# Kernel optimization log

Measured on AMD Instinct MI355X. Metric: run time of the kernel, lower is better.

Reference implementation:

```python
import jax, jax.numpy as jnp
import numpy as np

N = 50000      # nodes
F_IN = 500     # in_channels
MID = 64       # mid_layer_channel
H = 2          # heads
OUT = 40       # out_channels
E = 800000     # edges per order
ORDER = 3
NEG_SLOPE = 0.2


def _gat(x, edge_index, W, a_src, a_dst, b, concat):
    # PyG-style GATConv (eval mode, dropout off), with self loops.
    n = x.shape[0]
    heads, ch = a_src.shape
    h = (x @ W).reshape(n, heads, ch)                    # [N,H,C]
    loop = jnp.arange(n)
    src = jnp.concatenate([edge_index[0], loop])
    dst = jnp.concatenate([edge_index[1], loop])
    al_s = jnp.sum(h * a_src, axis=-1)                   # [N,H]
    al_d = jnp.sum(h * a_dst, axis=-1)                   # [N,H]
    e = jax.nn.leaky_relu(al_s[src] + al_d[dst], NEG_SLOPE)   # [Etot,H]
    m = jax.ops.segment_max(e, dst, num_segments=n)      # softmax over incoming edges per dst
    ex = jnp.exp(e - m[dst])
    den = jax.ops.segment_sum(ex, dst, num_segments=n)
    alpha = ex / (den[dst] + 1e-16)
    out = jax.ops.segment_sum(alpha[:, :, None] * h[src], dst, num_segments=n)  # [N,H,C]
    if concat:
        return out.reshape(n, heads * ch) + b
    return out.mean(axis=1) + b


def _aggr(states, Wmix, wfin):
    # NOrderAggrConv (depth=2): mix order states with [order,order] weights + ELU,
    # then reduce to a single state with a learned [order] combination.
    h = jnp.stack(states, axis=1)                        # [N,order,C]
    h = jax.nn.elu(jnp.einsum('nkc,kj->njc', h, Wmix))
    return jnp.einsum('nkc,k->nc', h, wfin)


def setup_inputs():
    key = jax.random.key(0)
    ks = jax.random.split(key, 40)
    d = {}
    d['node_feature'] = jax.random.normal(ks[0], (N, F_IN), jnp.float32)
    for o in range(ORDER):
        d[f'adj{o}'] = jax.random.randint(ks[1 + o], (2, E), 0, N)
    i = 4
    s = 0.05
    layer_dims = [(F_IN, MID, H * MID), (MID * H, OUT, OUT)]
    for l, (fin, c, bdim) in enumerate(layer_dims):
        for o in range(ORDER):
            d[f'W_{l}_{o}'] = jax.random.normal(ks[i], (fin, H * c), jnp.float32) * s; i += 1
            d[f'as_{l}_{o}'] = jax.random.normal(ks[i], (H, c), jnp.float32) * s; i += 1
            d[f'ad_{l}_{o}'] = jax.random.normal(ks[i], (H, c), jnp.float32) * s; i += 1
            d[f'b_{l}_{o}'] = jnp.zeros((bdim,), jnp.float32)
    for l in range(2):
        d[f'agg{l}_W'] = jax.random.normal(ks[i], (ORDER, ORDER), jnp.float32) * 0.5; i += 1
        d[f'agg{l}_w'] = jnp.full((ORDER,), 1.0 / ORDER, jnp.float32)
    return d


def reference(node_feature, adj0, adj1, adj2,
              W_0_0, as_0_0, ad_0_0, b_0_0,
              W_0_1, as_0_1, ad_0_1, b_0_1,
              W_0_2, as_0_2, ad_0_2, b_0_2,
              W_1_0, as_1_0, ad_1_0, b_1_0,
              W_1_1, as_1_1, ad_1_1, b_1_1,
              W_1_2, as_1_2, ad_1_2, b_1_2,
              agg0_W, agg0_w, agg1_W, agg1_w):
    adjs = (adj0, adj1, adj2)
    p0 = ((W_0_0, as_0_0, ad_0_0, b_0_0),
          (W_0_1, as_0_1, ad_0_1, b_0_1),
          (W_0_2, as_0_2, ad_0_2, b_0_2))
    p1 = ((W_1_0, as_1_0, ad_1_0, b_1_0),
          (W_1_1, as_1_1, ad_1_1, b_1_1),
          (W_1_2, as_1_2, ad_1_2, b_1_2))
    aggs = ((agg0_W, agg0_w), (agg1_W, agg1_w))
    x = node_feature  # eval mode: dropout is identity
    for l, params in enumerate((p0, p1)):
        concat = (l == 0)
        states = [jax.nn.elu(_gat(x, adjs[o], *params[o], concat)) for o in range(ORDER)]
        x = _aggr(states, *aggs[l])
    return jax.nn.log_softmax(x, axis=1)
```

## Files before the change

### kernel.cpp

```cpp
#include <hip/hip_runtime.h>
#include <cstdint>
#include <cstddef>
#include <math.h>


typedef __attribute__((ext_vector_type(8))) short short8;
typedef __attribute__((ext_vector_type(4))) float f32x4;
typedef __attribute__((ext_vector_type(2))) float f32x2;

struct P3f { const float* p[3]; };
struct P3c { const int* p[3]; };

#define SSEG 8
#define SEGSH 17

__device__ __forceinline__ float leakyf(float x) { return x > 0.f ? x : 0.2f * x; }
__device__ __forceinline__ float eluf(float x)   { return x > 0.f ? x : expm1f(x); }

__device__ __forceinline__ unsigned short bf16r(float x) {
  unsigned int u = __float_as_uint(x);
  u += 0x7fffu + ((u >> 16) & 1u);
  return (unsigned short)(u >> 16);
}
__device__ __forceinline__ float bflo(unsigned int u) { return __uint_as_float(u << 16); }
__device__ __forceinline__ float bfhi(unsigned int u) { return __uint_as_float(u & 0xffff0000u); }

__device__ __forceinline__ void bf8_fma2(uint4 q, float xx, f32x2* a) {
  f32x2 v0 = {bflo(q.x), bfhi(q.x)};
  f32x2 v1 = {bflo(q.y), bfhi(q.y)};
  f32x2 v2 = {bflo(q.z), bfhi(q.z)};
  f32x2 v3 = {bflo(q.w), bfhi(q.w)};
  a[0] += xx * v0;
  a[1] += xx * v1;
  a[2] += xx * v2;
  a[3] += xx * v3;
}

__global__ __launch_bounds__(256) void zero_int_kernel(int* p, int n) {
  int i = blockIdx.x * blockDim.x + threadIdx.x;
  if (i < n) p[i] = 0;
}

__global__ __launch_bounds__(256) void convA_kernel(const float* __restrict__ A,
    unsigned short* __restrict__ Ab, int M, int K, int Kpad) {
  int i = blockIdx.x * blockDim.x + threadIdx.x;
  int row = i >> 6;
  int koff = (i & 63) * 8;
  if (row >= M) return;
  const float* ap = A + (size_t)row * K;
  unsigned short v[8];
  if (koff + 8 <= K) {
    float4 q0 = ((const float4*)(ap + koff))[0];
    float4 q1 = ((const float4*)(ap + koff))[1];
    v[0] = bf16r(q0.x); v[1] = bf16r(q0.y); v[2] = bf16r(q0.z); v[3] = bf16r(q0.w);
    v[4] = bf16r(q1.x); v[5] = bf16r(q1.y); v[6] = bf16r(q1.z); v[7] = bf16r(q1.w);
  } else {
#pragma unroll
    for (int k = 0; k < 8; ++k)
      v[k] = (koff + k < K) ? bf16r(ap[koff + k]) : (unsigned short)0;
  }
  *(uint4*)(Ab + (size_t)row * Kpad + koff) = *(const uint4*)v;
}

__global__ __launch_bounds__(256) void count3_kernel(P3c adj,
    int* __restrict__ segcnt, int* __restrict__ posb, int E, int N) {
  int i = blockIdx.x * blockDim.x + threadIdx.x;
  int o = blockIdx.y;
  if (i < E) {
    int d = adj.p[o][E + i];
    int s = i >> SEGSH;
    if (s > SSEG - 1) s = SSEG - 1;
    posb[(size_t)o * E + i] = atomicAdd(&segcnt[((size_t)o * SSEG + s) * N + d], 1);
  }
}

__global__ __launch_bounds__(256) void nodeseg_scan_kernel(int* __restrict__ segcnt,
    int* __restrict__ cntb, int N) {
  int n = blockIdx.x * blockDim.x + threadIdx.x;
  int o = blockIdx.y;
  if (n >= N) return;
  int run = 0;
#pragma unroll
  for (int s = 0; s < SSEG; ++s) {
    size_t idx = ((size_t)o * SSEG + s) * N + n;
    int c = segcnt[idx];
    segcnt[idx] = run;
    run += c;
  }
  cntb[o * N + n] = run;
}

#define SCAN_T 256
#define SCAN_VPT 8
#define SCAN_TILE 2048

__global__ __launch_bounds__(SCAN_T) void scan1_kernel(const int* __restrict__ cntb,
    int* __restrict__ rowptrb, int* __restrict__ bsums, int N) {
  __shared__ int lds[SCAN_T];
  const int o = blockIdx.y;
  const int* cnt = cntb + o * N;
  int* rowptr = rowptrb + o * (N + 1);
  int t = threadIdx.x;
  int base = blockIdx.x * SCAN_TILE + t * SCAN_VPT;
  int v[SCAN_VPT];
  int s = 0;
#pragma unroll
  for (int i = 0; i < SCAN_VPT; ++i) {
    int idx = base + i;
    int x = (idx < N) ? cnt[idx] : 0;
    s += x;
    v[i] = s;
  }
  lds[t] = s;
  __syncthreads();
  for (int off = 1; off < SCAN_T; off <<= 1) {
    int add = (t >= off) ? lds[t - off] : 0;
    __syncthreads();
    lds[t] += add;
    __syncthreads();
  }
  int excl = (t > 0) ? lds[t - 1] : 0;
#pragma unroll
  for (int i = 0; i < SCAN_VPT; ++i) {
    int idx = base + i;
    if (idx < N) rowptr[idx + 1] = excl + v[i];
  }
  if (t == SCAN_T - 1) bsums[o * 64 + blockIdx.x] = lds[t];
}

__global__ void scan2_kernel(int* bsums, int nb, int* rowptrb, int N) {
  if (threadIdx.x == 0 && blockIdx.x == 0) {
    for (int o = 0; o < 3; ++o) {
      int run = 0;
      for (int i = 0; i < nb; ++i) {
        int x = bsums[o * 64 + i];
        bsums[o * 64 + i] = run;
        run += x;
      }
      rowptrb[o * (N + 1)] = 0;
    }
  }
}

__global__ __launch_bounds__(256) void scan3_kernel(int* __restrict__ rowptrb,
    const int* __restrict__ bsums, int N) {
  int idx = blockIdx.x * blockDim.x + threadIdx.x;
  int o = blockIdx.y;
  if (idx < N) rowptrb[o * (N + 1) + idx + 1] += bsums[o * 64 + idx / SCAN_TILE];
}

__global__ __launch_bounds__(256) void fill3_kernel(P3c adj,
    const int* __restrict__ rowptrb, const int* __restrict__ segcnt,
    const int* __restrict__ posb, int* __restrict__ colvb, int E, int N) {
  int i = blockIdx.x * blockDim.x + threadIdx.x;
  int o = blockIdx.y;
  if (i < E) {
    const int* a = adj.p[o];
    int d = a[E + i];
    int s = i >> SEGSH;
    if (s > SSEG - 1) s = SSEG - 1;
    int pos = segcnt[((size_t)o * SSEG + s) * N + d] + posb[(size_t)o * E + i];
    colvb[(size_t)o * E + rowptrb[o * (N + 1) + d] + pos] = a[i];
  }
}

__global__ __launch_bounds__(256) void alpha3_kernel(const int* __restrict__ rowptrB,
    const int* __restrict__ colvB, const float2* __restrict__ alsB,
    const float2* __restrict__ aldB, float2* __restrict__ alphB, int N, int E) {
  int w = blockIdx.x * blockDim.x + threadIdx.x;
  int o = blockIdx.y;
  if (w >= N) return;
  const int* rowptr = rowptrB + o * (N + 1);
  const int* colv = colvB + (size_t)o * E;
  const float2* als = alsB + (size_t)o * N;
  const float2 b = (aldB + (size_t)o * N)[w];
  float2* alph = alphB + (size_t)o * E;
  const int beg = rowptr[w], end = rowptr[w + 1];
  for (int j = beg; j < end; ++j) {
    int s = colv[j];
    float2 a = als[s];
    alph[j] = make_float2(__expf(leakyf(a.x + b.x)), __expf(leakyf(a.y + b.y)));
  }
}

__global__ __launch_bounds__(256) void conv_bt3_kernel(P3f W,
    unsigned short* __restrict__ BtB, int K, int NC, int Kpad) {
  int n = blockIdx.y;
  int o = blockIdx.z;
  int k = blockIdx.x * 256 + threadIdx.x;
  if (k >= Kpad) return;
  float v = (k < K) ? W.p[o][(size_t)k * NC + n] : 0.f;
  BtB[(size_t)o * NC * Kpad + (size_t)n * Kpad + k] = bf16r(v);
}

#define GBM 128
#define LDSTRIDE 40

template<int NT>
__global__ __launch_bounds__(256) void mfma_gemm_kernel(
    const unsigned short* __restrict__ Ab, const unsigned short* __restrict__ BtB,
    P3f asp, P3f adp, unsigned short* __restrict__ CbB,
    float2* __restrict__ alsB, float2* __restrict__ aldB, int M, int Kpad) {
  constexpr int NC = NT * 16;
  constexpr int CH = NT * 8;
  __shared__ unsigned short As[GBM * LDSTRIDE];
  __shared__ unsigned short Bs[NC * LDSTRIDE];
  const int t = threadIdx.x;
  const int o = blockIdx.y;
  const int wave = t >> 6, lane = t & 63;
  const int quad = lane >> 4, l16 = lane & 15;
  const int m0 = blockIdx.x * GBM;
  const unsigned short* Bt = BtB + (size_t)o * NC * Kpad;
  unsigned short* Cb = CbB + (size_t)o * M * NC;
  float2* al_s = alsB + (size_t)o * M;
  float2* al_d = aldB + (size_t)o * M;
  const float* a_src = asp.p[o];
  const float* a_dst = adp.p[o];

  f32x4 acc[2][NT];
#pragma unroll
  for (int i = 0; i < 2; ++i)
#pragma unroll
    for (int j = 0; j < NT; ++j) acc[i][j] = (f32x4){0.f, 0.f, 0.f, 0.f};

  const int arow = t >> 1;
  const int akoff = (t & 1) * 16;
  const int gm = m0 + arow;
  const unsigned short* arowp = Ab + (size_t)gm * Kpad;
  const unsigned short* browp = Bt + (size_t)arow * Kpad;

  for (int k0 = 0; k0 < Kpad; k0 += 32) {
    if (k0) __syncthreads();
    const int kb = k0 + akoff;
    {
      uint4 q0 = {0, 0, 0, 0}, q1 = {0, 0, 0, 0};
      if (gm < M) {
        const uint4* p = (const uint4*)(arowp + kb);
        q0 = p[0]; q1 = p[1];
      }
      short8* dst = (short8*)&As[arow * LDSTRIDE + akoff];
      union { uint4 q; short8 s; } c0, c1;
      c0.q = q0; c1.q = q1;
      dst[0] = c0.s;
      dst[1] = c1.s;
    }
    if (arow < NC) {
      const uint4* p = (const uint4*)(browp + kb);
      uint4 q0 = p[0], q1 = p[1];
      short8* dst = (short8*)&Bs[arow * LDSTRIDE + akoff];
      union { uint4 q; short8 s; } c0, c1;
      c0.q = q0; c1.q = q1;
      dst[0] = c0.s;
      dst[1] = c1.s;
    }
    __syncthreads();
    short8 af[2];
#pragma unroll
    for (int rt = 0; rt < 2; ++rt)
      af[rt] = *(const short8*)&As[(wave * 32 + rt * 16 + l16) * LDSTRIDE + quad * 8];
    short8 bfv[NT];
#pragma unroll
    for (int ct = 0; ct < NT; ++ct)
      bfv[ct] = *(const short8*)&Bs[(ct * 16 + l16) * LDSTRIDE + quad * 8];
#pragma unroll
    for (int rt = 0; rt < 2; ++rt)
#pragma unroll
      for (int ct = 0; ct < NT; ++ct)
        acc[rt][ct] = __builtin_amdgcn_mfma_f32_16x16x32_bf16(af[rt], bfv[ct],
                                                              acc[rt][ct], 0, 0, 0);
  }
  float asv[NT], adv[NT];
#pragma unroll
  for (int ct = 0; ct < NT; ++ct) {
    int col = ct * 16 + l16;
    asv[ct] = a_src[col];
    adv[ct] = a_dst[col];
  }
#pragma unroll
  for (int rt = 0; rt < 2; ++rt) {
    int gr0 = m0 + wave * 32 + rt * 16 + quad * 4;
#pragma unroll
    for (int r = 0; r < 4; ++r) {
      int gr = gr0 + r;
      float ps0 = 0.f, ps1 = 0.f, pd0 = 0.f, pd1 = 0.f;
#pragma unroll
      for (int ct = 0; ct < NT; ++ct) {
        int col = ct * 16 + l16;
        float v = acc[rt][ct][r];
        if (gr < M) Cb[(size_t)gr * NC + col] = bf16r(v);
        if (col < CH) { ps0 += v * asv[ct]; pd0 += v * adv[ct]; }
        else          { ps1 += v * asv[ct]; pd1 += v * adv[ct]; }
      }
#pragma unroll
      for (int off = 1; off < 16; off <<= 1) {
        ps0 += __shfl_xor(ps0, off, 64);
        ps1 += __shfl_xor(ps1, off, 64);
        pd0 += __shfl_xor(pd0, off, 64);
        pd1 += __shfl_xor(pd1, off, 64);
      }
      if (l16 == 0 && gr < M) {
        al_s[gr] = make_float2(ps0, ps1);
        al_d[gr] = make_float2(pd0, pd1);
      }
    }
  }
}

template<int C, int CONCAT>
__global__ __launch_bounds__(256) void gat_slot4_kernel(
    const unsigned short* __restrict__ hB, const float2* __restrict__ alsB,
    const float2* __restrict__ aldB, const int* __restrict__ rowptrB,
    const int* __restrict__ colvB, const float2* __restrict__ alphB,
    P3f biasp, unsigned short* __restrict__ outB, int N, int E) {
  constexpr int HC = 2 * C;
  constexpr int FLd = HC / 8;
  constexpr int HB = C / 8;
  constexpr int OW = CONCAT ? HC : C;
  const int o = blockIdx.y;
  const unsigned short* h = hB + (size_t)o * N * HC;
  const float2* al_s = alsB + (size_t)o * N;
  const float2* al_d = aldB + (size_t)o * N;
  const int* rowptr = rowptrB + o * (N + 1);
  const int* colv = colvB + (size_t)o * E;
  const float2* alph = alphB + (size_t)o * E;
  const float* bias = biasp.p[o];
  unsigned short* out = outB + (size_t)o * N * OW;

  const int gw = (blockIdx.x * blockDim.x + threadIdx.x) >> 6;
  const int lane = threadIdx.x & 63;
  const int slot = lane >> 4;
  const int f4 = lane & 15;
  const int w = gw * 4 + slot;
  if (gw * 4 >= N) return;
  const bool vn = w < N;
  const int wc = vn ? w : N - 1;
  const bool hl = f4 < FLd;

  const int beg = rowptr[wc];
  const int deg = vn ? (rowptr[wc + 1] - beg) : 0;
  int md = deg;
  md = max(md, __shfl_xor(md, 32, 64));
  md = max(md, __shfl_xor(md, 16, 64));

  const float2 ad = al_d[wc];
  const float2 asf = al_s[wc];
  const float xs0 = __expf(leakyf(asf.x + ad.x));
  const float xs1 = __expf(leakyf(asf.y + ad.y));
  float dp0 = xs0, dp1 = xs1;

  f32x2 acc[4] = {}, acc2[4] = {};
  if (hl) {
    uint4 q = ((const uint4*)(h + (size_t)wc * HC))[f4];
    bf8_fma2(q, (f4 < HB) ? xs0 : xs1, acc);
  }

  const float2 z2 = make_float2(0.f, 0.f);
  for (int t = 0; t < md; t += 4) {
    const int j0 = beg + t;
    const bool v0 = t < deg;
    const bool v1 = t + 1 < deg;
    const bool v2 = t + 2 < deg;
    const bool v3 = t + 3 < deg;
    const int s0 = v0 ? colv[j0] : 0;
    const int s1 = v1 ? colv[j0 + 1] : 0;
    const int s2 = v2 ? colv[j0 + 2] : 0;
    const int s3 = v3 ? colv[j0 + 3] : 0;
    const float2 a0 = v0 ? alph[j0] : z2;
    const float2 a1 = v1 ? alph[j0 + 1] : z2;
    const float2 a2 = v2 ? alph[j0 + 2] : z2;
    const float2 a3 = v3 ? alph[j0 + 3] : z2;
    uint4 q0 = make_uint4(0, 0, 0, 0), q1 = q0, q2 = q0, q3 = q0;
    if (v0 && hl) q0 = ((const uint4*)(h + (size_t)s0 * HC))[f4];
    if (v1 && hl) q1 = ((const uint4*)(h + (size_t)s1 * HC))[f4];
    if (v2 && hl) q2 = ((const uint4*)(h + (size_t)s2 * HC))[f4];
    if (v3 && hl) q3 = ((const uint4*)(h + (size_t)s3 * HC))[f4];
    dp0 += (a0.x + a1.x) + (a2.x + a3.x);
    dp1 += (a0.y + a1.y) + (a2.y + a3.y);
    if (v0 && hl) bf8_fma2(q0, (f4 < HB) ? a0.x : a0.y, acc);
    if (v1 && hl) bf8_fma2(q1, (f4 < HB) ? a1.x : a1.y, acc2);
    if (v2 && hl) bf8_fma2(q2, (f4 < HB) ? a2.x : a2.y, acc);
    if (v3 && hl) bf8_fma2(q3, (f4 < HB) ? a3.x : a3.y, acc2);
  }
#pragma unroll
  for (int i = 0; i < 4; ++i) acc[i] += acc2[i];

  const float inv0 = 1.f / (dp0 + 1e-16f), inv1 = 1.f / (dp1 + 1e-16f);
  if (CONCAT) {
    if (vn && hl) {
      const float xx = (f4 < HB) ? inv0 : inv1;
      const float* bp = bias + f4 * 8;
      unsigned int pk[4];
#pragma unroll
      for (int i = 0; i < 4; ++i) {
        unsigned short lo = bf16r(eluf(acc[i][0] * xx + bp[2 * i]));
        unsigned short hi = bf16r(eluf(acc[i][1] * xx + bp[2 * i + 1]));
        pk[i] = (unsigned int)lo | ((unsigned int)hi << 16);
      }
      ((uint4*)(out + (size_t)w * OW + f4 * 8))[0] = make_uint4(pk[0], pk[1], pk[2], pk[3]);
    }
  } else {
    float p[8];
#pragma unroll
    for (int i = 0; i < 4; ++i) {
      p[2 * i]     = __shfl(acc[i][0], lane + HB, 64);
      p[2 * i + 1] = __shfl(acc[i][1], lane + HB, 64);
    }
    if (vn && f4 < HB) {
      const float* bp = bias + f4 * 8;
      unsigned int pk[4];
#pragma unroll
      for (int i = 0; i < 4; ++i) {
        float v0 = 0.5f * (acc[i][0] * inv0 + p[2 * i] * inv1) + bp[2 * i];
        float v1 = 0.5f * (acc[i][1] * inv0 + p[2 * i + 1] * inv1) + bp[2 * i + 1];
        pk[i] = (unsigned int)bf16r(eluf(v0)) | ((unsigned int)bf16r(eluf(v1)) << 16);
      }
      ((uint4*)(out + (size_t)w * OW + f4 * 8))[0] = make_uint4(pk[0], pk[1], pk[2], pk[3]);
    }
  }
}

template<int BF16OUT>
__global__ __launch_bounds__(256) void mixb_kernel(const unsigned short* __restrict__ sb,
    const float* __restrict__ Wm, const float* __restrict__ wf,
    void* __restrict__ out, int perU) {
  int i = blockIdx.x * blockDim.x + threadIdx.x;
  if (i >= perU) return;
  const unsigned int* sp = (const unsigned int*)sb;
  unsigned int u0 = sp[i];
  unsigned int u1 = sp[perU + i];
  unsigned int u2 = sp[2 * perU + i];
  float a0 = bflo(u0), a1 = bfhi(u0);
  float b0 = bflo(u1), b1 = bfhi(u1);
  float c0 = bflo(u2), c1 = bfhi(u2);
  float r0 = 0.f, r1 = 0.f;
#pragma unroll
  for (int j = 0; j < 3; ++j) {
    float w0 = Wm[j], w1 = Wm[3 + j], w2 = Wm[6 + j], wj = wf[j];
    r0 += wj * eluf(a0 * w0 + b0 * w1 + c0 * w2);
    r1 += wj * eluf(a1 * w0 + b1 * w1 + c1 * w2);
  }
  if (BF16OUT) {
    ((unsigned int*)out)[i] = (unsigned int)bf16r(r0) | ((unsigned int)bf16r(r1) << 16);
  } else {
    ((float2*)out)[i] = make_float2(r0, r1);
  }
}

__global__ __launch_bounds__(256) void log_softmax_kernel(const float* __restrict__ x,
    float* __restrict__ out, int N, int C) {
  int w = (blockIdx.x * blockDim.x + threadIdx.x) >> 6;
  int lane = threadIdx.x & 63;
  if (w >= N) return;
  float v = (lane < C) ? x[(size_t)w * C + lane] : -INFINITY;
  float mx = v;
#pragma unroll
  for (int off = 1; off < 64; off <<= 1) mx = fmaxf(mx, __shfl_xor(mx, off, 64));
  float ex = (lane < C) ? expf(v - mx) : 0.f;
  float s = ex;
#pragma unroll
  for (int off = 1; off < 64; off <<= 1) s += __shfl_xor(s, off, 64);
  if (lane < C) out[(size_t)w * C + lane] = v - mx - logf(s);
}

extern "C" void kernel_launch(void* const* d_in, const int* in_sizes, int n_in,
                              void* d_out, int out_size, void* d_ws, size_t ws_size,
                              hipStream_t stream) {
  const int F_IN = 500;
  const int N = in_sizes[0] / F_IN;
  const int E = in_sizes[1] / 2;
  const int HC0 = 128;
  const int HC1 = 80;
  const int C1 = 40;
  const int K0pad = 512, K1pad = 128;

  const float* x0 = (const float*)d_in[0];
  P3c adj;
  adj.p[0] = (const int*)d_in[1];
  adj.p[1] = (const int*)d_in[2];
  adj.p[2] = (const int*)d_in[3];
  P3f W0p, as0p, ad0p, b0p, W1p, as1p, ad1p, b1p;
  for (int o = 0; o < 3; ++o) {
    W0p.p[o]  = (const float*)d_in[4 + 4 * o + 0];
    as0p.p[o] = (const float*)d_in[4 + 4 * o + 1];
    ad0p.p[o] = (const float*)d_in[4 + 4 * o + 2];
    b0p.p[o]  = (const float*)d_in[4 + 4 * o + 3];
    W1p.p[o]  = (const float*)d_in[16 + 4 * o + 0];
    as1p.p[o] = (const float*)d_in[16 + 4 * o + 1];
    ad1p.p[o] = (const float*)d_in[16 + 4 * o + 2];
    b1p.p[o]  = (const float*)d_in[16 + 4 * o + 3];
  }
  const float* agg0W = (const float*)d_in[28];
  const float* agg0w = (const float*)d_in[29];
  const float* agg1W = (const float*)d_in[30];
  const float* agg1w = (const float*)d_in[31];

  char* ws = (char*)d_ws;
  size_t off = 0;
  auto alloc = [&](size_t bytes) -> void* {
    off = (off + 255) & ~(size_t)255;
    void* p = ws + off;
    off += bytes;
    return p;
  };
  int* rowptrb = (int*)alloc((size_t)3 * (N + 1) * 4);
  int* colvb   = (int*)alloc((size_t)3 * E * 4);
  int* cntb    = (int*)alloc((size_t)3 * N * 4);
  int* bsums   = (int*)alloc(3 * 64 * 4);
  unsigned short* x0b = (unsigned short*)alloc((size_t)N * K0pad * 2);
  unsigned short* hB  = (unsigned short*)alloc((size_t)3 * N * HC0 * 2);
  unsigned short* stB = (unsigned short*)alloc((size_t)3 * N * HC0 * 2);
  float* x2 = (float*)alloc((size_t)N * C1 * 4);
  float2* alsB = (float2*)alloc((size_t)3 * N * 8);
  float2* aldB = (float2*)alloc((size_t)3 * N * 8);
  unsigned short* Bt0B = (unsigned short*)alloc((size_t)3 * HC0 * K0pad * 2);
  unsigned short* Bt1B = (unsigned short*)alloc((size_t)3 * HC1 * K1pad * 2);
  float2* alphb = (float2*)x0b;
  int* posb   = (int*)hB;
  int* segcnt = (int*)stB;
  (void)ws_size;

  const int TB = 256;
  const int nbE = (E + TB - 1) / TB;
  const int nbN = (N + TB - 1) / TB;
  const int scanBlocks = (N + SCAN_TILE - 1) / SCAN_TILE;
  const int gemmBlocks = (N + GBM - 1) / GBM;
  const int slot4Blocks = (int)(((size_t)((N + 3) / 4) * 64 + TB - 1) / TB);
  const int lsBlocks = (int)(((size_t)N * 64 + TB - 1) / TB);

  convA_kernel<<<(int)(((size_t)N * 64 + TB - 1) / TB), TB, 0, stream>>>(
      x0, x0b, N, F_IN, K0pad);
  conv_bt3_kernel<<<dim3((K0pad + 255) / 256, HC0, 3), TB, 0, stream>>>(W0p, Bt0B, F_IN, HC0, K0pad);
  conv_bt3_kernel<<<dim3((K1pad + 255) / 256, HC1, 3), TB, 0, stream>>>(W1p, Bt1B, HC0, HC1, K1pad);

  zero_int_kernel<<<(3 * SSEG * N + TB - 1) / TB, TB, 0, stream>>>(segcnt, 3 * SSEG * N);
  count3_kernel<<<dim3(nbE, 3), TB, 0, stream>>>(adj, segcnt, posb, E, N);
  nodeseg_scan_kernel<<<dim3(nbN, 3), TB, 0, stream>>>(segcnt, cntb, N);
  scan1_kernel<<<dim3(scanBlocks, 3), SCAN_T, 0, stream>>>(cntb, rowptrb, bsums, N);
  scan2_kernel<<<1, 64, 0, stream>>>(bsums, scanBlocks, rowptrb, N);
  scan3_kernel<<<dim3(nbN, 3), TB, 0, stream>>>(rowptrb, bsums, N);
  fill3_kernel<<<dim3(nbE, 3), TB, 0, stream>>>(adj, rowptrb, segcnt, posb, colvb, E, N);

  mfma_gemm_kernel<8><<<dim3(gemmBlocks, 3), TB, 0, stream>>>(
      x0b, Bt0B, as0p, ad0p, hB, alsB, aldB, N, K0pad);
  alpha3_kernel<<<dim3(nbN, 3), TB, 0, stream>>>(rowptrb, colvb, alsB, aldB, alphb, N, E);
  gat_slot4_kernel<64, 1><<<dim3(slot4Blocks, 3), TB, 0, stream>>>(
      hB, alsB, aldB, rowptrb, colvb, alphb, b0p, stB, N, E);
  mixb_kernel<1><<<((N * HC0 / 2) + TB - 1) / TB, TB, 0, stream>>>(
      stB, agg0W, agg0w, stB, N * HC0 / 2);

  mfma_gemm_kernel<5><<<dim3(gemmBlocks, 3), TB, 0, stream>>>(
      stB, Bt1B, as1p, ad1p, hB, alsB, aldB, N, K1pad);
  alpha3_kernel<<<dim3(nbN, 3), TB, 0, stream>>>(rowptrb, colvb, alsB, aldB, alphb, N, E);
  gat_slot4_kernel<40, 0><<<dim3(slot4Blocks, 3), TB, 0, stream>>>(
      hB, alsB, aldB, rowptrb, colvb, alphb, b1p, stB, N, E);
  mixb_kernel<0><<<((N * C1 / 2) + TB - 1) / TB, TB, 0, stream>>>(
      stB, agg1W, agg1w, x2, N * C1 / 2);

  log_softmax_kernel<<<lsBlocks, TB, 0, stream>>>(x2, (float*)d_out, N, C1);
}
```

Before: 816.4 us.

## Sort destination nodes by degree to balance GAT aggregation wavefronts

Adds a counting sort of nodes by in-degree (histogram, scan, scatter) that produces a permutation for each order. The GAT aggregation kernel then processes nodes in permuted order, so the four nodes sharing a wavefront have similar degrees and less time is lost waiting on the largest degree. The cost is three extra small kernels plus an indirect lookup. Output writes also become non-contiguous, and neighbouring slots no longer touch adjacent rows.

Measured after the change: 825.4 us. Within noise of the previous version (+1.1%).

```diff
diff --git a/kernel.cpp b/kernel.cpp
--- a/kernel.cpp
+++ b/kernel.cpp
@@ -13,6 +13,7 @@
 
 #define SSEG 8
 #define SEGSH 17
+#define NBIN 128
 
 __device__ __forceinline__ float leakyf(float x) { return x > 0.f ? x : 0.2f * x; }
 __device__ __forceinline__ float eluf(float x)   { return x > 0.f ? x : expm1f(x); }
@@ -162,6 +163,58 @@
     int pos = segcnt[((size_t)o * SSEG + s) * N + d] + posb[(size_t)o * E + i];
     colvb[(size_t)o * E + rowptrb[o * (N + 1) + d] + pos] = a[i];
   }
+}
+
+__global__ __launch_bounds__(256) void hist3_kernel(const int* __restrict__ rowptrb,
+    int* __restrict__ binhist, int N) {
+  __shared__ int lh[NBIN];
+  const int o = blockIdx.y;
+  const int t = threadIdx.x;
+  if (t < NBIN) lh[t] = 0;
+  __syncthreads();
+  int n = blockIdx.x * 256 + t;
+  if (n < N) {
+    const int* rowptr = rowptrb + o * (N + 1);
+    int deg = rowptr[n + 1] - rowptr[n];
+    int b = deg < NBIN ? deg : NBIN - 1;
+    atomicAdd(&lh[b], 1);
+  }
+  __syncthreads();
+  if (t < NBIN && lh[t]) atomicAdd(&binhist[o * NBIN + t], lh[t]);
+}
+
+__global__ void binscan_kernel(const int* __restrict__ binhist,
+    int* __restrict__ binctr) {
+  int o = threadIdx.x;
+  if (o < 3) {
+    int run = 0;
+    for (int b = 0; b < NBIN; ++b) {
+      binctr[o * NBIN + b] = run;
+      run += binhist[o * NBIN + b];
+    }
+  }
+}
+
+__global__ __launch_bounds__(256) void scatter3_kernel(const int* __restrict__ rowptrb,
+    int* __restrict__ binctr, int* __restrict__ permb, int N) {
+  __shared__ int lh[NBIN];
+  __shared__ int lbase[NBIN];
+  const int o = blockIdx.y;
+  const int t = threadIdx.x;
+  if (t < NBIN) lh[t] = 0;
+  __syncthreads();
+  int n = blockIdx.x * 256 + t;
+  int b = 0, lr = 0;
+  if (n < N) {
+    const int* rowptr = rowptrb + o * (N + 1);
+    int deg = rowptr[n + 1] - rowptr[n];
+    b = deg < NBIN ? deg : NBIN - 1;
+    lr = atomicAdd(&lh[b], 1);
+  }
+  __syncthreads();
+  if (t < NBIN && lh[t]) lbase[t] = atomicAdd(&binctr[o * NBIN + t], lh[t]);
+  __syncthreads();
+  if (n < N) permb[(size_t)o * N + lbase[b] + lr] = n;
 }
 
 __global__ __launch_bounds__(256) void alpha3_kernel(const int* __restrict__ rowptrB,
@@ -311,7 +364,8 @@
     const unsigned short* __restrict__ hB, const float2* __restrict__ alsB,
     const float2* __restrict__ aldB, const int* __restrict__ rowptrB,
     const int* __restrict__ colvB, const float2* __restrict__ alphB,
-    P3f biasp, unsigned short* __restrict__ outB, int N, int E) {
+    const int* __restrict__ permB, P3f biasp, unsigned short* __restrict__ outB,
+    int N, int E) {
   constexpr int HC = 2 * C;
   constexpr int FLd = HC / 8;
   constexpr int HB = C / 8;
@@ -323,6 +377,7 @@
   const int* rowptr = rowptrB + o * (N + 1);
   const int* colv = colvB + (size_t)o * E;
   const float2* alph = alphB + (size_t)o * E;
+  const int* perm = permB + (size_t)o * N;
   const float* bias = biasp.p[o];
   unsigned short* out = outB + (size_t)o * N * OW;
 
@@ -333,7 +388,7 @@
   const int w = gw * 4 + slot;
   if (gw * 4 >= N) return;
   const bool vn = w < N;
-  const int wc = vn ? w : N - 1;
+  const int wc = perm[vn ? w : N - 1];
   const bool hl = f4 < FLd;
 
   const int beg = rowptr[wc];
@@ -396,7 +451,7 @@
         unsigned short hi = bf16r(eluf(acc[i][1] * xx + bp[2 * i + 1]));
         pk[i] = (unsigned int)lo | ((unsigned int)hi << 16);
       }
-      ((uint4*)(out + (size_t)w * OW + f4 * 8))[0] = make_uint4(pk[0], pk[1], pk[2], pk[3]);
+      ((uint4*)(out + (size_t)wc * OW + f4 * 8))[0] = make_uint4(pk[0], pk[1], pk[2], pk[3]);
     }
   } else {
     float p[8];
@@ -414,7 +469,7 @@
         float v1 = 0.5f * (acc[i][1] * inv0 + p[2 * i + 1] * inv1) + bp[2 * i + 1];
         pk[i] = (unsigned int)bf16r(eluf(v0)) | ((unsigned int)bf16r(eluf(v1)) << 16);
       }
-      ((uint4*)(out + (size_t)w * OW + f4 * 8))[0] = make_uint4(pk[0], pk[1], pk[2], pk[3]);
+      ((uint4*)(out + (size_t)wc * OW + f4 * 8))[0] = make_uint4(pk[0], pk[1], pk[2], pk[3]);
     }
   }
 }
@@ -506,6 +561,9 @@
   int* colvb   = (int*)alloc((size_t)3 * E * 4);
   int* cntb    = (int*)alloc((size_t)3 * N * 4);
   int* bsums   = (int*)alloc(3 * 64 * 4);
+  int* permb   = (int*)alloc((size_t)3 * N * 4);
+  int* binhist = (int*)alloc(3 * NBIN * 4);
+  int* binctr  = (int*)alloc(3 * NBIN * 4);
   unsigned short* x0b = (unsigned short*)alloc((size_t)N * K0pad * 2);
   unsigned short* hB  = (unsigned short*)alloc((size_t)3 * N * HC0 * 2);
   unsigned short* stB = (unsigned short*)alloc((size_t)3 * N * HC0 * 2);
@@ -533,18 +591,22 @@
   conv_bt3_kernel<<<dim3((K1pad + 255) / 256, HC1, 3), TB, 0, stream>>>(W1p, Bt1B, HC0, HC1, K1pad);
 
   zero_int_kernel<<<(3 * SSEG * N + TB - 1) / TB, TB, 0, stream>>>(segcnt, 3 * SSEG * N);
+  zero_int_kernel<<<(3 * NBIN + TB - 1) / TB, TB, 0, stream>>>(binhist, 3 * NBIN);
   count3_kernel<<<dim3(nbE, 3), TB, 0, stream>>>(adj, segcnt, posb, E, N);
   nodeseg_scan_kernel<<<dim3(nbN, 3), TB, 0, stream>>>(segcnt, cntb, N);
   scan1_kernel<<<dim3(scanBlocks, 3), SCAN_T, 0, stream>>>(cntb, rowptrb, bsums, N);
   scan2_kernel<<<1, 64, 0, stream>>>(bsums, scanBlocks, rowptrb, N);
   scan3_kernel<<<dim3(nbN, 3), TB, 0, stream>>>(rowptrb, bsums, N);
   fill3_kernel<<<dim3(nbE, 3), TB, 0, stream>>>(adj, rowptrb, segcnt, posb, colvb, E, N);
+  hist3_kernel<<<dim3(nbN, 3), TB, 0, stream>>>(rowptrb, binhist, N);
+  binscan_kernel<<<1, 64, 0, stream>>>(binhist, binctr);
+  scatter3_kernel<<<dim3(nbN, 3), TB, 0, stream>>>(rowptrb, binctr, permb, N);
 
   mfma_gemm_kernel<8><<<dim3(gemmBlocks, 3), TB, 0, stream>>>(
       x0b, Bt0B, as0p, ad0p, hB, alsB, aldB, N, K0pad);
   alpha3_kernel<<<dim3(nbN, 3), TB, 0, stream>>>(rowptrb, colvb, alsB, aldB, alphb, N, E);
   gat_slot4_kernel<64, 1><<<dim3(slot4Blocks, 3), TB, 0, stream>>>(
-      hB, alsB, aldB, rowptrb, colvb, alphb, b0p, stB, N, E);
+      hB, alsB, aldB, rowptrb, colvb, alphb, permb, b0p, stB, N, E);
   mixb_kernel<1><<<((N * HC0 / 2) + TB - 1) / TB, TB, 0, stream>>>(
       stB, agg0W, agg0w, stB, N * HC0 / 2);
 
@@ -552,7 +614,7 @@
       stB, Bt1B, as1p, ad1p, hB, alsB, aldB, N, K1pad);
   alpha3_kernel<<<dim3(nbN, 3), TB, 0, stream>>>(rowptrb, colvb, alsB, aldB, alphb, N, E);
   gat_slot4_kernel<40, 0><<<dim3(slot4Blocks, 3), TB, 0, stream>>>(
-      hB, alsB, aldB, rowptrb, colvb, alphb, b1p, stB, N, E);
+      hB, alsB, aldB, rowptrb, colvb, alphb, permb, b1p, stB, N, E);
   mixb_kernel<0><<<((N * C1 / 2) + TB - 1) / TB, TB, 0, stream>>>(
       stB, agg1W, agg1w, x2, N * C1 / 2);
 
```

## Fuse layer-0 GEMM with edge counting in one heterogeneous launch

Applied to the files above, without the earlier changes.

Layer-0 MFMA GEMM blocks and edge-count atomic blocks are interleaved in a single grid, one GEMM block per nine, so the memory- and atomic-bound counting overlaps the compute-bound GEMM instead of running as separate launches. The GEMM body moves into a device function shared by both kernels. Workspace aliasing changes so posb and segcnt live in stB rather than hB, since hB is now written concurrently by the GEMM. This adds block-index arithmetic, and the fused kernel's register and LDS use applies to the count blocks, which may reduce occupancy.

New measurement: 778.0 us. 4.7% less time.

```diff
diff --git a/kernel.cpp b/kernel.cpp
--- a/kernel.cpp
+++ b/kernel.cpp
@@ -197,19 +197,15 @@
 #define LDSTRIDE 40
 
 template<int NT>
-__global__ __launch_bounds__(256) void mfma_gemm_kernel(
+__device__ __forceinline__ void gemm_body(int m0, int o, int t,
     const unsigned short* __restrict__ Ab, const unsigned short* __restrict__ BtB,
     P3f asp, P3f adp, unsigned short* __restrict__ CbB,
-    float2* __restrict__ alsB, float2* __restrict__ aldB, int M, int Kpad) {
+    float2* __restrict__ alsB, float2* __restrict__ aldB, int M, int Kpad,
+    unsigned short* As, unsigned short* Bs) {
   constexpr int NC = NT * 16;
   constexpr int CH = NT * 8;
-  __shared__ unsigned short As[GBM * LDSTRIDE];
-  __shared__ unsigned short Bs[NC * LDSTRIDE];
-  const int t = threadIdx.x;
-  const int o = blockIdx.y;
   const int wave = t >> 6, lane = t & 63;
   const int quad = lane >> 4, l16 = lane & 15;
-  const int m0 = blockIdx.x * GBM;
   const unsigned short* Bt = BtB + (size_t)o * NC * Kpad;
   unsigned short* Cb = CbB + (size_t)o * M * NC;
   float2* al_s = alsB + (size_t)o * M;
@@ -302,6 +298,46 @@
         al_s[gr] = make_float2(ps0, ps1);
         al_d[gr] = make_float2(pd0, pd1);
       }
+    }
+  }
+}
+
+template<int NT>
+__global__ __launch_bounds__(256) void mfma_gemm_kernel(
+    const unsigned short* __restrict__ Ab, const unsigned short* __restrict__ BtB,
+    P3f asp, P3f adp, unsigned short* __restrict__ CbB,
+    float2* __restrict__ alsB, float2* __restrict__ aldB, int M, int Kpad) {
+  __shared__ unsigned short As[GBM * LDSTRIDE];
+  __shared__ unsigned short Bs[NT * 16 * LDSTRIDE];
+  gemm_body<NT>(blockIdx.x * GBM, blockIdx.y, threadIdx.x,
+                Ab, BtB, asp, adp, CbB, alsB, aldB, M, Kpad, As, Bs);
+}
+
+__global__ __launch_bounds__(256) void gemm0_count_kernel(
+    const unsigned short* __restrict__ Ab, const unsigned short* __restrict__ BtB,
+    P3f asp, P3f adp, unsigned short* __restrict__ CbB,
+    float2* __restrict__ alsB, float2* __restrict__ aldB, int M, int Kpad,
+    P3c adj, int* __restrict__ segcnt, int* __restrict__ posb, int E, int N,
+    int nbG) {
+  __shared__ unsigned short As[GBM * LDSTRIDE];
+  __shared__ unsigned short Bs[128 * LDSTRIDE];
+  const int x = blockIdx.x;
+  const int o = blockIdx.y;
+  const int gx = x / 9;
+  const int rem = x - gx * 9;
+  if (rem == 0 && gx < nbG) {
+    gemm_body<8>(gx * GBM, o, threadIdx.x,
+                 Ab, BtB, asp, adp, CbB, alsB, aldB, M, Kpad, As, Bs);
+  } else {
+    int nG = (x + 8) / 9;
+    if (nG > nbG) nG = nbG;
+    const int c = x - nG;
+    const int i = c * 256 + threadIdx.x;
+    if (i < E) {
+      int d = adj.p[o][E + i];
+      int s = i >> SEGSH;
+      if (s > SSEG - 1) s = SSEG - 1;
+      posb[(size_t)o * E + i] = atomicAdd(&segcnt[((size_t)o * SSEG + s) * N + d], 1);
     }
   }
 }
@@ -515,8 +551,8 @@
   unsigned short* Bt0B = (unsigned short*)alloc((size_t)3 * HC0 * K0pad * 2);
   unsigned short* Bt1B = (unsigned short*)alloc((size_t)3 * HC1 * K1pad * 2);
   float2* alphb = (float2*)x0b;
-  int* posb   = (int*)hB;
-  int* segcnt = (int*)stB;
+  int* posb   = (int*)stB;
+  int* segcnt = (int*)(stB + (size_t)3 * E * 2);
   (void)ws_size;
 
   const int TB = 256;
@@ -533,15 +569,22 @@
   conv_bt3_kernel<<<dim3((K1pad + 255) / 256, HC1, 3), TB, 0, stream>>>(W1p, Bt1B, HC0, HC1, K1pad);
 
   zero_int_kernel<<<(3 * SSEG * N + TB - 1) / TB, TB, 0, stream>>>(segcnt, 3 * SSEG * N);
-  count3_kernel<<<dim3(nbE, 3), TB, 0, stream>>>(adj, segcnt, posb, E, N);
+  if (8 * gemmBlocks >= nbE) {
+    gemm0_count_kernel<<<dim3(gemmBlocks * 9, 3), TB, 0, stream>>>(
+        x0b, Bt0B, as0p, ad0p, hB, alsB, aldB, N, K0pad,
+        adj, segcnt, posb, E, N, gemmBlocks);
+  } else {
+    count3_kernel<<<dim3(nbE, 3), TB, 0, stream>>>(adj, segcnt, posb, E, N);
+    mfma_gemm_kernel<8><<<dim3(gemmBlocks, 3), TB, 0, stream>>>(
+        x0b, Bt0B, as0p, ad0p, hB, alsB, aldB, N, K0pad);
+  }
+
   nodeseg_scan_kernel<<<dim3(nbN, 3), TB, 0, stream>>>(segcnt, cntb, N);
   scan1_kernel<<<dim3(scanBlocks, 3), SCAN_T, 0, stream>>>(cntb, rowptrb, bsums, N);
   scan2_kernel<<<1, 64, 0, stream>>>(bsums, scanBlocks, rowptrb, N);
   scan3_kernel<<<dim3(nbN, 3), TB, 0, stream>>>(rowptrb, bsums, N);
   fill3_kernel<<<dim3(nbE, 3), TB, 0, stream>>>(adj, rowptrb, segcnt, posb, colvb, E, N);
 
-  mfma_gemm_kernel<8><<<dim3(gemmBlocks, 3), TB, 0, stream>>>(
-      x0b, Bt0B, as0p, ad0p, hB, alsB, aldB, N, K0pad);
   alpha3_kernel<<<dim3(nbN, 3), TB, 0, stream>>>(rowptrb, colvb, alsB, aldB, alphb, N, E);
   gat_slot4_kernel<64, 1><<<dim3(slot4Blocks, 3), TB, 0, stream>>>(
       hB, alsB, aldB, rowptrb, colvb, alphb, b0p, stB, N, E);
```
